# Performance work log

Hardware: AMD Instinct MI355X
Metric: run time of the kernel (lower is better)

The kernel has to match this reference:

```python
import jax, jax.numpy as jnp
import numpy as np

LR = 0.01        # memory update learning rate (init kwarg lr)
INIT_SCALE = 0.01
B, N, D = 8, 1024, 256


def setup_inputs() -> dict:
    key = jax.random.key(0)
    k1, k2, k3, k4, k5 = jax.random.split(key, 5)
    return {
        "sequence": jax.random.normal(k1, (B, N, D), dtype=jnp.float32),
        "targets": jax.random.normal(k2, (B, N, D), dtype=jnp.float32),
        "theta0": jax.random.normal(k3, (D, D), dtype=jnp.float32) * INIT_SCALE,
        "W_e": jax.random.normal(k4, (D, D), dtype=jnp.float32) * INIT_SCALE,
        "W_o": jax.random.normal(k5, (D, D), dtype=jnp.float32) * INIT_SCALE,
    }


def reference(sequence, targets, theta0, W_e, W_o):
    # process_sequence on (batch, n, d) with targets: theta is reset to theta0
    # for each batch element, then updated sequentially per token (delta rule).
    def step(theta, xt):
        x_t, tgt_t = xt                      # (d,), (d,)
        h = W_e @ x_t                        # encode: F.linear(x, W_e)
        pred = theta @ h                     # predict with current memory
        err = tgt_t - pred
        theta_new = theta + LR * jnp.outer(err, h)   # rank-1 fast-weight update
        out = W_o @ pred                     # output projection of PREDICTION
        return theta_new, out

    def per_batch(seq_b, tgt_b):             # (n, d), (n, d)
        _, outs = jax.lax.scan(step, theta0, (seq_b, tgt_b))
        return outs                          # (n, d)

    return jax.vmap(per_batch)(sequence, targets)   # (batch, n, d)
```

## Files before the change

kernel.cpp:

```cpp
#include <hip/hip_runtime.h>

#define LR_C 0.01f
#define NB 8
#define NTOK 1024
#define DD 256
#define CH 8
#define NCHUNK (NTOK / CH)

#define DPP_ADD(x, ctrl) \
    ((x) + __int_as_float(__builtin_amdgcn_update_dpp( \
        0, __float_as_int(x), (ctrl), 0xF, 0xF, true)))

#define REDUCE_ALL64(s) do { \
    s = DPP_ADD(s, 0xB1); \
    s = DPP_ADD(s, 0x4E); \
    s = DPP_ADD(s, 0x141); \
    s = DPP_ADD(s, 0x140); \
    s += __shfl_xor(s, 16, 64); \
    s += __shfl_xor(s, 32, 64); \
} while (0)

__device__ __forceinline__ void gload16(const float* g, float* l) {
    __builtin_amdgcn_global_load_lds(
        (const __attribute__((address_space(1))) unsigned int*)g,
        (__attribute__((address_space(3))) unsigned int*)l, 16, 0, 0);
}
__device__ __forceinline__ void gload4(const float* g, float* l) {
    __builtin_amdgcn_global_load_lds(
        (const __attribute__((address_space(1))) unsigned int*)g,
        (__attribute__((address_space(3))) unsigned int*)l, 4, 0, 0);
}

#define GM 128
#define GN 64
#define GK 16

__global__ __launch_bounds__(512) void gemm_abt_kernel(
    const float* __restrict__ A, const float* __restrict__ B,
    float* __restrict__ C)
{
    __shared__ float As[GK][GM + 4];
    __shared__ float Bs[GK][GN + 4];
    const int t    = threadIdx.x;
    const int arow = t >> 2, ak = (t & 3) * 4;
    const int brow = t >> 2, bk = (t & 3) * 4;
    const int tx   = t & 15, ty = t >> 4;

    const float* Ap = A + (size_t)(blockIdx.x * GM + arow) * DD + ak;
    const float* Bp = B + (size_t)(blockIdx.y * GN + (t < 256 ? brow : 0)) * DD + bk;

    float4 acc[4];
    #pragma unroll
    for (int i = 0; i < 4; ++i) acc[i] = make_float4(0.f, 0.f, 0.f, 0.f);

    float4 a0 = *reinterpret_cast<const float4*>(Ap);
    float4 b0 = *reinterpret_cast<const float4*>(Bp);

    for (int k0 = 0; k0 < DD; k0 += GK) {
        __syncthreads();
        As[ak + 0][arow] = a0.x; As[ak + 1][arow] = a0.y;
        As[ak + 2][arow] = a0.z; As[ak + 3][arow] = a0.w;
        if (t < 256) {
            Bs[bk + 0][brow] = b0.x; Bs[bk + 1][brow] = b0.y;
            Bs[bk + 2][brow] = b0.z; Bs[bk + 3][brow] = b0.w;
        }
        __syncthreads();
        if (k0 + GK < DD) {
            a0 = *reinterpret_cast<const float4*>(Ap + k0 + GK);
            b0 = *reinterpret_cast<const float4*>(Bp + k0 + GK);
        }
        #pragma unroll
        for (int k = 0; k < GK; ++k) {
            float4 av = *reinterpret_cast<const float4*>(&As[k][ty * 4]);
            float4 bv = *reinterpret_cast<const float4*>(&Bs[k][tx * 4]);
            acc[0].x = fmaf(av.x, bv.x, acc[0].x); acc[0].y = fmaf(av.x, bv.y, acc[0].y);
            acc[0].z = fmaf(av.x, bv.z, acc[0].z); acc[0].w = fmaf(av.x, bv.w, acc[0].w);
            acc[1].x = fmaf(av.y, bv.x, acc[1].x); acc[1].y = fmaf(av.y, bv.y, acc[1].y);
            acc[1].z = fmaf(av.y, bv.z, acc[1].z); acc[1].w = fmaf(av.y, bv.w, acc[1].w);
            acc[2].x = fmaf(av.z, bv.x, acc[2].x); acc[2].y = fmaf(av.z, bv.y, acc[2].y);
            acc[2].z = fmaf(av.z, bv.z, acc[2].z); acc[2].w = fmaf(av.z, bv.w, acc[2].w);
            acc[3].x = fmaf(av.w, bv.x, acc[3].x); acc[3].y = fmaf(av.w, bv.y, acc[3].y);
            acc[3].z = fmaf(av.w, bv.z, acc[3].z); acc[3].w = fmaf(av.w, bv.w, acc[3].w);
        }
    }
    #pragma unroll
    for (int i = 0; i < 4; ++i) {
        float* cp = C + (size_t)(blockIdx.x * GM + ty * 4 + i) * DD
                      + blockIdx.y * GN + tx * 4;
        *reinterpret_cast<float4*>(cp) = acc[i];
    }
}

__global__ __launch_bounds__(512) void gemm_pt_kernel(
    const float* __restrict__ PT, const float* __restrict__ B,
    float* __restrict__ C)
{
    __shared__ float As[GK][GM + 4];
    __shared__ float Bs[GK][GN + 4];
    const int t  = threadIdx.x;
    const int mb = blockIdx.x;
    const int b  = mb >> 3;
    const int t0 = (mb & 7) * GM;

    const int krow = t >> 5, tcol = (t & 31) * 4;
    const int brow = t >> 2, bk   = (t & 3) * 4;
    const int tx   = t & 15, ty   = t >> 4;

    const float* Ap = PT + (size_t)b * DD * NTOK + (size_t)krow * NTOK + t0 + tcol;
    const float* Bp = B + (size_t)(blockIdx.y * GN + (t < 256 ? brow : 0)) * DD + bk;

    float4 acc[4];
    #pragma unroll
    for (int i = 0; i < 4; ++i) acc[i] = make_float4(0.f, 0.f, 0.f, 0.f);

    float4 a0 = *reinterpret_cast<const float4*>(Ap);
    float4 b0 = *reinterpret_cast<const float4*>(Bp);

    for (int k0 = 0; k0 < DD; k0 += GK) {
        __syncthreads();
        *reinterpret_cast<float4*>(&As[krow][tcol]) = a0;
        if (t < 256) {
            Bs[bk + 0][brow] = b0.x; Bs[bk + 1][brow] = b0.y;
            Bs[bk + 2][brow] = b0.z; Bs[bk + 3][brow] = b0.w;
        }
        __syncthreads();
        if (k0 + GK < DD) {
            a0 = *reinterpret_cast<const float4*>(Ap + (size_t)(k0 + GK) * NTOK);
            b0 = *reinterpret_cast<const float4*>(Bp + k0 + GK);
        }
        #pragma unroll
        for (int k = 0; k < GK; ++k) {
            float4 av = *reinterpret_cast<const float4*>(&As[k][ty * 4]);
            float4 bv = *reinterpret_cast<const float4*>(&Bs[k][tx * 4]);
            acc[0].x = fmaf(av.x, bv.x, acc[0].x); acc[0].y = fmaf(av.x, bv.y, acc[0].y);
            acc[0].z = fmaf(av.x, bv.z, acc[0].z); acc[0].w = fmaf(av.x, bv.w, acc[0].w);
            acc[1].x = fmaf(av.y, bv.x, acc[1].x); acc[1].y = fmaf(av.y, bv.y, acc[1].y);
            acc[1].z = fmaf(av.y, bv.z, acc[1].z); acc[1].w = fmaf(av.y, bv.w, acc[1].w);
            acc[2].x = fmaf(av.z, bv.x, acc[2].x); acc[2].y = fmaf(av.z, bv.y, acc[2].y);
            acc[2].z = fmaf(av.z, bv.z, acc[2].z); acc[2].w = fmaf(av.z, bv.w, acc[2].w);
            acc[3].x = fmaf(av.w, bv.x, acc[3].x); acc[3].y = fmaf(av.w, bv.y, acc[3].y);
            acc[3].z = fmaf(av.w, bv.z, acc[3].z); acc[3].w = fmaf(av.w, bv.w, acc[3].w);
        }
    }
    #pragma unroll
    for (int i = 0; i < 4; ++i) {
        float* cp = C + (size_t)(b * NTOK + t0 + ty * 4 + i) * DD
                      + blockIdx.y * GN + tx * 4;
        *reinterpret_cast<float4*>(cp) = acc[i];
    }
}

__global__ __launch_bounds__(128) void gram_kernel(
    const float* __restrict__ H, float* __restrict__ Gram)
{
    const int blk  = blockIdx.x;
    const int b    = blk & 7;
    const int chk  = blk >> 3;
    const int w    = threadIdx.x >> 6;
    const int lane = threadIdx.x & 63;
    const float* Hc = H + ((size_t)b * NTOK + (size_t)chk * CH) * DD + lane * 4;

    float4 h[CH];
    #pragma unroll
    for (int i = 0; i < CH; ++i)
        h[i] = *reinterpret_cast<const float4*>(Hc + (size_t)i * DD);

    float sel = 0.f;
    #pragma unroll
    for (int i = 1; i < CH; ++i) {
        #pragma unroll
        for (int j = 0; j < i; ++j) {
            const int idx = i * (i - 1) / 2 + j;
            if ((idx & 1) == w) {
                float s = h[j].x * h[i].x;
                s = fmaf(h[j].y, h[i].y, s);
                s = fmaf(h[j].z, h[i].z, s);
                s = fmaf(h[j].w, h[i].w, s);
                REDUCE_ALL64(s);
                sel = (lane == idx) ? s : sel;
            }
        }
    }
    if (lane < 28 && (lane & 1) == w)
        Gram[((size_t)b * NCHUNK + chk) * 32 + lane] = sel;
}

__global__ __launch_bounds__(256, 2) void theta_scan_kernel(
    const float* __restrict__ H, const float* __restrict__ Tgt,
    const float* __restrict__ theta0, const float* __restrict__ Gram,
    float* __restrict__ PT)
{
    __shared__ float Hbuf[2][CH][DD];
    __shared__ float Scr[4][CH][64];
    __shared__ float TGb[2][64];
    __shared__ float GRb[2][64];

    const int b    = blockIdx.x & 7;
    const int rb   = blockIdx.x >> 3;
    const int wid  = threadIdx.x >> 6;
    const int lane = threadIdx.x & 63;
    const int row  = rb * 4 + wid;

    float4 th = *reinterpret_cast<const float4*>(
        theta0 + (size_t)row * DD + lane * 4);

    const float* Hb = H   + (size_t)b * NTOK * DD;
    const float* Tb = Tgt + (size_t)b * NTOK * DD;
    const float* Gb = Gram + (size_t)b * NCHUNK * 32;
    float*       Pb = PT  + ((size_t)b * DD + row) * NTOK;

    const int ll = lane & 31;
    const int tt = ll & 7, rr = ll >> 3;

    {
        const float* g0 = Hb + (size_t)(2 * wid) * DD + lane * 4;
        gload16(g0,      &Hbuf[0][2 * wid][0]);
        gload16(g0 + DD, &Hbuf[0][2 * wid + 1][0]);
        if (wid == 0)
            gload4(Tb + (size_t)tt * DD + rb * 4 + rr, &TGb[0][0]);
        if (wid == 1)
            gload4(Gb + ll, &GRb[0][0]);
    }

    for (int ch = 0; ch < NCHUNK; ++ch) {
        const int par = ch & 1;
        __syncthreads();

        if (ch + 1 < NCHUNK) {
            const int np = par ^ 1;
            const float* g0 = Hb + (size_t)((ch + 1) * CH + 2 * wid) * DD + lane * 4;
            gload16(g0,      &Hbuf[np][2 * wid][0]);
            gload16(g0 + DD, &Hbuf[np][2 * wid + 1][0]);
            if (wid == 0)
                gload4(Tb + (size_t)((ch + 1) * CH + tt) * DD + rb * 4 + rr,
                       &TGb[np][0]);
            if (wid == 1)
                gload4(Gb + (ch + 1) * 32 + ll, &GRb[np][0]);
        }

        float4 hh[CH]; float s[CH];
        #pragma unroll
        for (int i = 0; i < CH; ++i) {
            hh[i] = *reinterpret_cast<const float4*>(&Hbuf[par][i][lane * 4]);
            float sv = hh[i].x * th.x;
            sv = fmaf(hh[i].y, th.y, sv);
            sv = fmaf(hh[i].z, th.z, sv);
            sv = fmaf(hh[i].w, th.w, sv);
            s[i] = sv;
        }
        #pragma unroll
        for (int i = 0; i < CH; ++i) Scr[wid][i][lane] = s[i];
        const float* sb = &Scr[wid][0][0];
        float4 r0 = *reinterpret_cast<const float4*>(sb + lane * 8);
        float4 r1 = *reinterpret_cast<const float4*>(sb + lane * 8 + 4);
        float sum = ((r0.x + r0.y) + (r0.z + r0.w))
                  + ((r1.x + r1.y) + (r1.z + r1.w));
        sum = DPP_ADD(sum, 0xB1);
        sum = DPP_ADD(sum, 0x4E);
        sum = DPP_ADD(sum, 0x141);
        float a[CH];
        #pragma unroll
        for (int i = 0; i < CH; ++i)
            a[i] = __int_as_float(
                __builtin_amdgcn_readlane(__float_as_int(sum), 8 * i));

        const float4* tb4 = reinterpret_cast<const float4*>(&TGb[par][wid * 8]);
        float4 tg0 = tb4[0], tg1 = tb4[1];
        float lt[CH] = {LR_C * tg0.x, LR_C * tg0.y, LR_C * tg0.z, LR_C * tg0.w,
                        LR_C * tg1.x, LR_C * tg1.y, LR_C * tg1.z, LR_C * tg1.w};
        const float4* gb4 = reinterpret_cast<const float4*>(&GRb[par][0]);
        float gv[28];
        #pragma unroll
        for (int q = 0; q < 7; ++q)
            *reinterpret_cast<float4*>(&gv[q * 4]) = gb4[q];

        float e[CH], p[CH];
        #pragma unroll
        for (int i = 0; i < CH; ++i) {
            float pv = a[i];
            #pragma unroll
            for (int j = 0; j < i; ++j)
                pv = fmaf(e[j], gv[i * (i - 1) / 2 + j], pv);
            p[i] = pv;
            e[i] = fmaf(-LR_C, pv, lt[i]);
        }
        #pragma unroll
        for (int j = 0; j < CH; ++j) {
            th.x = fmaf(e[j], hh[j].x, th.x);
            th.y = fmaf(e[j], hh[j].y, th.y);
            th.z = fmaf(e[j], hh[j].z, th.z);
            th.w = fmaf(e[j], hh[j].w, th.w);
        }
        float sel = p[0];
        #pragma unroll
        for (int i = 1; i < CH; ++i) sel = (lane == i) ? p[i] : sel;
        if (lane < CH) Pb[ch * CH + lane] = sel;
    }
}

extern "C" void kernel_launch(void* const* d_in, const int* in_sizes, int n_in,
                              void* d_out, int out_size, void* d_ws, size_t ws_size,
                              hipStream_t stream) {
    const float* seq    = (const float*)d_in[0];
    const float* tgt    = (const float*)d_in[1];
    const float* theta0 = (const float*)d_in[2];
    const float* W_e    = (const float*)d_in[3];
    const float* W_o    = (const float*)d_in[4];
    float* out = (float*)d_out;

    float* Hbuf  = (float*)d_ws;
    float* PTbuf = Hbuf + (size_t)NB * NTOK * DD;
    float* Cbuf  = out;

    dim3 ggrid(NB * NTOK / GM, DD / GN);

    gemm_abt_kernel<<<ggrid, 512, 0, stream>>>(seq, W_e, Hbuf);
    gram_kernel<<<NB * NCHUNK, 128, 0, stream>>>(Hbuf, Cbuf);
    theta_scan_kernel<<<NB * 64, 256, 0, stream>>>(Hbuf, tgt, theta0, Cbuf, PTbuf);
    gemm_pt_kernel<<<ggrid, 512, 0, stream>>>(PTbuf, W_o, out);
}
```

Before: 216.3 us.

## Run theta scan with one wave per block, dropping block barriers

Restructures the theta scan so each block is a single 64-lane wave owning one theta row, with 2048 blocks instead of 512 four-wave blocks. Because the block is one wave, __syncthreads is removed and replaced by explicit vmcnt waits on the async global-to-LDS loads, with a manually unrolled double buffer. The dot-product reduction now does a full DPP/shuffle reduce per token instead of the LDS transpose scratch. The trade-offs are that each wave loads the full H chunk redundantly, and the correctness of the vmcnt(10) wait depends on how many loads are in flight.

After: 273.6 us. 26.5% more time.

```diff
diff --git a/kernel.cpp b/kernel.cpp
--- a/kernel.cpp
+++ b/kernel.cpp
@@ -185,116 +185,99 @@
         Gram[((size_t)b * NCHUNK + chk) * 32 + lane] = sel;
 }
 
-__global__ __launch_bounds__(256, 2) void theta_scan_kernel(
+#define STAGE_CHUNK(nc, pb) do { \
+    const float* hs_ = hbase + (size_t)(nc) * (CH * DD); \
+    gload16(hs_ + 0 * DD, &HB[pb][0][0]); \
+    gload16(hs_ + 1 * DD, &HB[pb][1][0]); \
+    gload16(hs_ + 2 * DD, &HB[pb][2][0]); \
+    gload16(hs_ + 3 * DD, &HB[pb][3][0]); \
+    gload16(hs_ + 4 * DD, &HB[pb][4][0]); \
+    gload16(hs_ + 5 * DD, &HB[pb][5][0]); \
+    gload16(hs_ + 6 * DD, &HB[pb][6][0]); \
+    gload16(hs_ + 7 * DD, &HB[pb][7][0]); \
+    gload4(tbase + (size_t)(nc) * (CH * DD), &TB[pb][0]); \
+    gload4(gbase + (size_t)(nc) * 32, &GB[pb][0]); \
+} while (0)
+
+#define SCAN_BODY(ch, par) do { \
+    const int nc_ = ((ch) + 1 < NCHUNK) ? (ch) + 1 : NCHUNK - 1; \
+    STAGE_CHUNK(nc_, (par) ^ 1); \
+     \
+    asm volatile("s_waitcnt vmcnt(10)" ::: "memory"); \
+    __builtin_amdgcn_sched_barrier(0); \
+    float4 hh[CH]; float s[CH]; \
+    _Pragma("unroll") \
+    for (int i_ = 0; i_ < CH; ++i_) { \
+        hh[i_] = *reinterpret_cast<const float4*>(&HB[par][i_][lane * 4]); \
+        float sv_ = hh[i_].x * th.x; \
+        sv_ = fmaf(hh[i_].y, th.y, sv_); \
+        sv_ = fmaf(hh[i_].z, th.z, sv_); \
+        sv_ = fmaf(hh[i_].w, th.w, sv_); \
+        s[i_] = sv_; \
+    } \
+    _Pragma("unroll") \
+    for (int i_ = 0; i_ < CH; ++i_) { REDUCE_ALL64(s[i_]); } \
+    float4 tg0_ = *reinterpret_cast<const float4*>(&TB[par][0]); \
+    float4 tg1_ = *reinterpret_cast<const float4*>(&TB[par][4]); \
+    float lt_[CH] = {LR_C * tg0_.x, LR_C * tg0_.y, LR_C * tg0_.z, LR_C * tg0_.w, \
+                     LR_C * tg1_.x, LR_C * tg1_.y, LR_C * tg1_.z, LR_C * tg1_.w}; \
+    float gv_[28]; \
+    _Pragma("unroll") \
+    for (int q_ = 0; q_ < 7; ++q_) \
+        *reinterpret_cast<float4*>(&gv_[q_ * 4]) = \
+            *reinterpret_cast<const float4*>(&GB[par][q_ * 4]); \
+    float e_[CH], p_[CH]; \
+    _Pragma("unroll") \
+    for (int i_ = 0; i_ < CH; ++i_) { \
+        float pv_ = s[i_]; \
+        _Pragma("unroll") \
+        for (int j_ = 0; j_ < i_; ++j_) \
+            pv_ = fmaf(e_[j_], gv_[i_ * (i_ - 1) / 2 + j_], pv_); \
+        p_[i_] = pv_; \
+        e_[i_] = fmaf(-LR_C, pv_, lt_[i_]); \
+    } \
+    _Pragma("unroll") \
+    for (int j_ = 0; j_ < CH; ++j_) { \
+        th.x = fmaf(e_[j_], hh[j_].x, th.x); \
+        th.y = fmaf(e_[j_], hh[j_].y, th.y); \
+        th.z = fmaf(e_[j_], hh[j_].z, th.z); \
+        th.w = fmaf(e_[j_], hh[j_].w, th.w); \
+    } \
+    float sel_ = p_[0]; \
+    _Pragma("unroll") \
+    for (int i_ = 1; i_ < CH; ++i_) sel_ = (lane == i_) ? p_[i_] : sel_; \
+    if (lane < CH) Pb[(ch) * CH + lane] = sel_; \
+} while (0)
+
+__global__ __launch_bounds__(64, 2) void theta_scan_kernel(
     const float* __restrict__ H, const float* __restrict__ Tgt,
     const float* __restrict__ theta0, const float* __restrict__ Gram,
     float* __restrict__ PT)
 {
-    __shared__ float Hbuf[2][CH][DD];
-    __shared__ float Scr[4][CH][64];
-    __shared__ float TGb[2][64];
-    __shared__ float GRb[2][64];
+    __shared__ float HB[2][CH][DD];
+    __shared__ float TB[2][64];
+    __shared__ float GB[2][64];
 
     const int b    = blockIdx.x & 7;
-    const int rb   = blockIdx.x >> 3;
-    const int wid  = threadIdx.x >> 6;
-    const int lane = threadIdx.x & 63;
-    const int row  = rb * 4 + wid;
+    const int row  = blockIdx.x >> 3;
+    const int lane = threadIdx.x;
 
     float4 th = *reinterpret_cast<const float4*>(
         theta0 + (size_t)row * DD + lane * 4);
-
-    const float* Hb = H   + (size_t)b * NTOK * DD;
-    const float* Tb = Tgt + (size_t)b * NTOK * DD;
-    const float* Gb = Gram + (size_t)b * NCHUNK * 32;
-    float*       Pb = PT  + ((size_t)b * DD + row) * NTOK;
-
-    const int ll = lane & 31;
-    const int tt = ll & 7, rr = ll >> 3;
-
-    {
-        const float* g0 = Hb + (size_t)(2 * wid) * DD + lane * 4;
-        gload16(g0,      &Hbuf[0][2 * wid][0]);
-        gload16(g0 + DD, &Hbuf[0][2 * wid + 1][0]);
-        if (wid == 0)
-            gload4(Tb + (size_t)tt * DD + rb * 4 + rr, &TGb[0][0]);
-        if (wid == 1)
-            gload4(Gb + ll, &GRb[0][0]);
-    }
-
-    for (int ch = 0; ch < NCHUNK; ++ch) {
-        const int par = ch & 1;
-        __syncthreads();
-
-        if (ch + 1 < NCHUNK) {
-            const int np = par ^ 1;
-            const float* g0 = Hb + (size_t)((ch + 1) * CH + 2 * wid) * DD + lane * 4;
-            gload16(g0,      &Hbuf[np][2 * wid][0]);
-            gload16(g0 + DD, &Hbuf[np][2 * wid + 1][0]);
-            if (wid == 0)
-                gload4(Tb + (size_t)((ch + 1) * CH + tt) * DD + rb * 4 + rr,
-                       &TGb[np][0]);
-            if (wid == 1)
-                gload4(Gb + (ch + 1) * 32 + ll, &GRb[np][0]);
-        }
-
-        float4 hh[CH]; float s[CH];
-        #pragma unroll
-        for (int i = 0; i < CH; ++i) {
-            hh[i] = *reinterpret_cast<const float4*>(&Hbuf[par][i][lane * 4]);
-            float sv = hh[i].x * th.x;
-            sv = fmaf(hh[i].y, th.y, sv);
-            sv = fmaf(hh[i].z, th.z, sv);
-            sv = fmaf(hh[i].w, th.w, sv);
-            s[i] = sv;
-        }
-        #pragma unroll
-        for (int i = 0; i < CH; ++i) Scr[wid][i][lane] = s[i];
-        const float* sb = &Scr[wid][0][0];
-        float4 r0 = *reinterpret_cast<const float4*>(sb + lane * 8);
-        float4 r1 = *reinterpret_cast<const float4*>(sb + lane * 8 + 4);
-        float sum = ((r0.x + r0.y) + (r0.z + r0.w))
-                  + ((r1.x + r1.y) + (r1.z + r1.w));
-        sum = DPP_ADD(sum, 0xB1);
-        sum = DPP_ADD(sum, 0x4E);
-        sum = DPP_ADD(sum, 0x141);
-        float a[CH];
-        #pragma unroll
-        for (int i = 0; i < CH; ++i)
-            a[i] = __int_as_float(
-                __builtin_amdgcn_readlane(__float_as_int(sum), 8 * i));
-
-        const float4* tb4 = reinterpret_cast<const float4*>(&TGb[par][wid * 8]);
-        float4 tg0 = tb4[0], tg1 = tb4[1];
-        float lt[CH] = {LR_C * tg0.x, LR_C * tg0.y, LR_C * tg0.z, LR_C * tg0.w,
-                        LR_C * tg1.x, LR_C * tg1.y, LR_C * tg1.z, LR_C * tg1.w};
-        const float4* gb4 = reinterpret_cast<const float4*>(&GRb[par][0]);
-        float gv[28];
-        #pragma unroll
-        for (int q = 0; q < 7; ++q)
-            *reinterpret_cast<float4*>(&gv[q * 4]) = gb4[q];
-
-        float e[CH], p[CH];
-        #pragma unroll
-        for (int i = 0; i < CH; ++i) {
-            float pv = a[i];
-            #pragma unroll
-            for (int j = 0; j < i; ++j)
-                pv = fmaf(e[j], gv[i * (i - 1) / 2 + j], pv);
-            p[i] = pv;
-            e[i] = fmaf(-LR_C, pv, lt[i]);
-        }
-        #pragma unroll
-        for (int j = 0; j < CH; ++j) {
-            th.x = fmaf(e[j], hh[j].x, th.x);
-            th.y = fmaf(e[j], hh[j].y, th.y);
-            th.z = fmaf(e[j], hh[j].z, th.z);
-            th.w = fmaf(e[j], hh[j].w, th.w);
-        }
-        float sel = p[0];
-        #pragma unroll
-        for (int i = 1; i < CH; ++i) sel = (lane == i) ? p[i] : sel;
-        if (lane < CH) Pb[ch * CH + lane] = sel;
+    asm volatile("s_waitcnt vmcnt(0)" ::: "memory");
+
+    const float* hbase = H    + (size_t)b * NTOK * DD + lane * 4;
+    const float* tbase = Tgt  + (size_t)b * NTOK * DD + row
+                              + (size_t)(lane & 7) * DD;
+    const float* gbase = Gram + (size_t)b * NCHUNK * 32 + (lane & 31);
+    float*       Pb    = PT   + ((size_t)b * DD + row) * NTOK;
+
+    STAGE_CHUNK(0, 0);
+
+    #pragma clang loop unroll(disable)
+    for (int ch = 0; ch < NCHUNK; ch += 2) {
+        SCAN_BODY(ch, 0);
+        SCAN_BODY(ch + 1, 1);
     }
 }
 
@@ -316,6 +299,6 @@
 
     gemm_abt_kernel<<<ggrid, 512, 0, stream>>>(seq, W_e, Hbuf);
     gram_kernel<<<NB * NCHUNK, 128, 0, stream>>>(Hbuf, Cbuf);
-    theta_scan_kernel<<<NB * 64, 256, 0, stream>>>(Hbuf, tgt, theta0, Cbuf, PTbuf);
+    theta_scan_kernel<<<NB * 256, 64, 0, stream>>>(Hbuf, tgt, theta0, Cbuf, PTbuf);
     gemm_pt_kernel<<<ggrid, 512, 0, stream>>>(PTbuf, W_o, out);
 }
```
